# Optimization experiments

Hardware: AMD Instinct MI355X
Metric: run time of the kernel (lower is better)

## Reference

```python
import jax, jax.numpy as jnp
import numpy as np

N = 16384
MUL0, MUL1, MUL2 = 128, 64, 32            # multiplicities of 0e, 1e, 2e
A = 16                                    # node_attr_dim (Ax0e)
D0, D1, D2 = MUL0, MUL1 * 3, MUL2 * 5     # e3nn flat block sizes
DIN = D0 + D1 + D2                        # 480
NGATE = MUL1 + MUL2                       # 96 gate scalars
OUT0 = MUL0 + NGATE                       # 224 scalar (0e) outputs of fctp_1


def setup_inputs() -> dict:
    key = jax.random.key(0)
    ks = jax.random.split(key, 10)
    f32 = jnp.float32
    return {
        "node_vec": jax.random.normal(ks[0], (N, DIN), f32),
        "node_embedding": jax.random.normal(ks[1], (N, A), f32),
        # fctp_1 path weights (fully-connected TP with Ax0e attr)
        "W1_l0": jax.random.normal(ks[2], (MUL0, A, OUT0), f32),
        "W1_l1": jax.random.normal(ks[3], (MUL1, A, MUL1), f32),
        "W1_l2": jax.random.normal(ks[4], (MUL2, A, MUL2), f32),
        "b1": jnp.zeros((OUT0,), f32),
        # fctp_2 scalar-path weight (only 0e x 0e -> 0e path exists)
        "W2": jax.random.normal(ks[5], (MUL0, A, A), f32),
        "b2": jnp.zeros((A,), f32),
        # scalar readout MLP: LinearRS -> SiLU -> LinearRS
        "W3": jax.random.normal(ks[6], (A, A), f32),
        "b3": jnp.zeros((A,), f32),
        "W4": jax.random.normal(ks[7], (A, 1), f32),
        "b4": jnp.zeros((1,), f32),
    }


def reference(node_vec, node_embedding, W1_l0, W1_l1, W1_l2, b1, W2, b2, W3, b3, W4, b4):
    # split e3nn-layout features into per-l blocks [N, mul, 2l+1]
    x0 = node_vec[:, :D0]                               # [N, 128]   l=0
    x1 = node_vec[:, D0:D0 + D1].reshape(-1, MUL1, 3)   # [N, 64, 3] l=1
    x2 = node_vec[:, D0 + D1:].reshape(-1, MUL2, 5)     # [N, 32, 5] l=2
    a = node_embedding                                  # [N, A] 0e scalars
    # fctp_1: fully-connected TP with Ax0e attr -> per-l bilinear mix (path-normalized)
    s = jnp.einsum('ni,na,iak->nk', x0, a, W1_l0) / np.sqrt(MUL0 * A) + b1  # [N, 224]
    y1 = jnp.einsum('nim,na,iak->nkm', x1, a, W1_l1) / np.sqrt(MUL1 * A)    # [N, 64, 3]
    y2 = jnp.einsum('nim,na,iak->nkm', x2, a, W1_l2) / np.sqrt(MUL2 * A)    # [N, 32, 5]
    # SwishGate: SiLU on scalars, sigmoid gates multiply the l>0 channels
    scalars = jax.nn.silu(s[:, :MUL0])
    gates = jax.nn.sigmoid(s[:, MUL0:])
    y1 = y1 * gates[:, :MUL1, None]
    y2 = y2 * gates[:, MUL1:, None]
    # fctp_2: output irreps = Ax0e, so only the 0e x 0e -> 0e path exists;
    # the gated l>0 features have no path to 0e (same as the torch TP).
    mid = jnp.einsum('ni,na,iak->nk', scalars, a, W2) / np.sqrt(MUL0 * A) + b2  # [N, A]
    # output_network: LinearRS -> SiLU -> LinearRS (rescale 1/sqrt(fan_in))
    h = jax.nn.silu(mid @ W3 / np.sqrt(A) + b3)
    return h @ W4 / np.sqrt(A) + b4                     # [N, 1]
```

## Files before the change

kernel.cpp:

```cpp
#include <hip/hip_runtime.h>
#include <hip/hip_bf16.h>


#define NKC 64

typedef _Float16 h8  __attribute__((ext_vector_type(8)));
typedef _Float16 h2  __attribute__((ext_vector_type(2)));
typedef float    f32x4 __attribute__((ext_vector_type(4)));

static __device__ __forceinline__ unsigned int pack2h(float a, float b) {
    h2 t = {(_Float16)a, (_Float16)b};
    return __builtin_bit_cast(unsigned int, t);
}
static __device__ __forceinline__ f32x4 mfma_h(uint4 a, uint4 b, f32x4 c) {
    return __builtin_amdgcn_mfma_f32_16x16x32_f16(
        __builtin_bit_cast(h8, a), __builtin_bit_cast(h8, b), c, 0, 0, 0);
}
static __device__ __forceinline__ uint4 mk_afrag(_Float16 xh, const h2* ee) {
    h2 xx = {xh, xh};
    uint4 r;
    r.x = __builtin_bit_cast(unsigned int, (h2)(xx * ee[0]));
    r.y = __builtin_bit_cast(unsigned int, (h2)(xx * ee[1]));
    r.z = __builtin_bit_cast(unsigned int, (h2)(xx * ee[2]));
    r.w = __builtin_bit_cast(unsigned int, (h2)(xx * ee[3]));
    return r;
}

__global__ __launch_bounds__(256) void prep_kernel(
        const float* __restrict__ W1, const float* __restrict__ W2,
        _Float16* __restrict__ W1T, _Float16* __restrict__ W2T) {
    const int b = blockIdx.x, kc = b >> 2, tp = b & 3;
    const int tid = threadIdx.x;
    __shared__ float l1[32 * 36];
    __shared__ float l2[32 * 20];

    {
        int row = tid >> 3, c4 = tid & 7;
        float4 v = *(const float4*)(W1 + (size_t)(kc * 32 + row) * 224 + tp * 32 + c4 * 4);
        *(float4*)(l1 + row * 36 + c4 * 4) = v;
    }
    if (tp == 0 && tid < 128) {
        int row = tid >> 2, c4 = tid & 3;
        float4 v = *(const float4*)(W2 + (size_t)(kc * 32 + row) * 16 + c4 * 4);
        *(float4*)(l2 + row * 20 + c4 * 4) = v;
    }
    __syncthreads();

    if (tid < 128) {
        int tl = tid >> 6, t = tp * 2 + tl, lane = tid & 63;
        int q = lane >> 4, cc = lane & 15, colL = tl * 16 + cc;
        unsigned int w[4];
#pragma unroll
        for (int jj = 0; jj < 4; ++jj)
            w[jj] = pack2h(l1[(q * 8 + 2 * jj) * 36 + colL],
                           l1[(q * 8 + 2 * jj + 1) * 36 + colL]);
        *(uint4*)(W1T + (size_t)kc * 4096 + (t * 64 + lane) * 8) =
            make_uint4(w[0], w[1], w[2], w[3]);
    }
    if (tp == 0 && tid >= 128 && tid < 192) {
        int lane = tid - 128, q = lane >> 4, cc = lane & 15;
        unsigned int w[4];
#pragma unroll
        for (int jj = 0; jj < 4; ++jj)
            w[jj] = pack2h(l2[(q * 8 + 2 * jj) * 20 + cc],
                           l2[(q * 8 + 2 * jj + 1) * 20 + cc]);
        *(uint4*)(W2T + (size_t)kc * 512 + lane * 8) = make_uint4(w[0], w[1], w[2], w[3]);
    }
}

__global__ __launch_bounds__(1024, 4) void main_kernel(
        const float* __restrict__ node_vec, const float* __restrict__ emb,
        const _Float16* __restrict__ W1T, const _Float16* __restrict__ W2T,
        const float* __restrict__ b1, const float* __restrict__ b2,
        const float* __restrict__ W3, const float* __restrict__ b3,
        const float* __restrict__ W4, const float* __restrict__ b4,
        float* __restrict__ out) {
    const int tid  = threadIdx.x;
    const int wave = tid >> 6, lane = tid & 63;
    const int q = lane >> 4, c = lane & 15;
    const int ihalf = q >> 1;
    const int g = wave >> 2;
    const int cs = wave & 3;
    const int nodeBase = blockIdx.x * 64;

    __shared__ _Float16 x0s[64 * 136];
    __shared__ _Float16 scs[64 * 136];
    __shared__ float    midp[4 * 64 * 17];
    __shared__ float    mids[64 * 17];
    __shared__ float    w3s[256];
    __shared__ float    b3s[16];
    __shared__ float    w4s[16];
    __shared__ float    b4s[1];

    for (int idx = tid; idx < 2048; idx += 1024) {
        int row = idx >> 5, c4 = idx & 31;
        float4 v = *(const float4*)(node_vec + (size_t)(nodeBase + row) * 480 + c4 * 4);
        unsigned int ua = pack2h(v.x, v.y), ub = pack2h(v.z, v.w);
        *(uint2*)(&x0s[row * 136 + c4 * 4]) = make_uint2(ua, ub);
    }
    if (tid < 256) w3s[tid] = W3[tid];
    if (tid < 16) { b3s[tid] = b3[tid]; w4s[tid] = W4[tid]; }
    if (tid == 0) b4s[0] = b4[0];

    h2 ee[4];
    {
        const float* ep = emb + (size_t)(nodeBase + g * 16 + c) * 16 + (q & 1) * 8;
        float4 v0 = *(const float4*)ep;
        float4 v1 = *(const float4*)(ep + 4);
        ee[0] = (h2){(_Float16)v0.x, (_Float16)v0.y};
        ee[1] = (h2){(_Float16)v0.z, (_Float16)v0.w};
        ee[2] = (h2){(_Float16)v1.x, (_Float16)v1.y};
        ee[3] = (h2){(_Float16)v1.z, (_Float16)v1.w};
    }
    __syncthreads();

    f32x4 acc[2];
    acc[0] = (f32x4){0.f, 0.f, 0.f, 0.f};
    acc[1] = (f32x4){0.f, 0.f, 0.f, 0.f};

    const int rowA = g * 16 + c;
    const uint4* bptr = (const uint4*)W1T + lane;
    const int cs2 = cs * 2;

    uint4 bb0[2], bb1[2];
    _Float16 xs0, xs1;
    bb0[0] = bptr[(cs2    ) * 64];
    bb0[1] = bptr[(cs2 + 1) * 64];
    xs0 = x0s[rowA * 136 + ihalf];

    for (int kc = 0; kc < NKC; kc += 2) {
        const int k1 = kc + 1;
        bb1[0] = bptr[(k1 * 8 + cs2    ) * 64];
        bb1[1] = bptr[(k1 * 8 + cs2 + 1) * 64];
        xs1 = x0s[rowA * 136 + 2 * k1 + ihalf];
        {
            uint4 af = mk_afrag(xs0, ee);
            acc[0] = mfma_h(af, bb0[0], acc[0]);
            acc[1] = mfma_h(af, bb0[1], acc[1]);
        }
        const int k2 = (kc + 2 < NKC) ? kc + 2 : 0;
        bb0[0] = bptr[(k2 * 8 + cs2    ) * 64];
        bb0[1] = bptr[(k2 * 8 + cs2 + 1) * 64];
        xs0 = x0s[rowA * 136 + 2 * k2 + ihalf];
        {
            uint4 af = mk_afrag(xs1, ee);
            acc[0] = mfma_h(af, bb1[0], acc[0]);
            acc[1] = mfma_h(af, bb1[1], acc[1]);
        }
    }

    const float inv2048 = 0.022097086912079608f;
#pragma unroll
    for (int tt = 0; tt < 2; ++tt) {
        int t = cs2 + tt;
        float bb1v = b1[t * 16 + c];
#pragma unroll
        for (int r = 0; r < 4; ++r) {
            int node = g * 16 + q * 4 + r;
            float s  = acc[tt][r] * inv2048 + bb1v;
            float sc = s / (1.f + __expf(-s));
            scs[node * 136 + t * 16 + c] = (_Float16)sc;
        }
    }
    __syncthreads();

    {
        const int ks = cs;
        const int rowS = g * 16 + c;
        const uint4* b2p = (const uint4*)W2T + lane;
        f32x4 macc = (f32x4){0.f, 0.f, 0.f, 0.f};
        const int kb = ks * 16;
        uint4 wb0, wb1;
        _Float16 sv0, sv1;
        wb0 = b2p[kb * 64];
        sv0 = scs[rowS * 136 + 2 * kb + ihalf];
        for (int u = 0; u < 16; u += 2) {
            const int kB = kb + u + 1;
            wb1 = b2p[kB * 64];
            sv1 = scs[rowS * 136 + 2 * kB + ihalf];
            macc = mfma_h(mk_afrag(sv0, ee), wb0, macc);
            const int kC = (u + 2 < 16) ? kb + u + 2 : kb;
            wb0 = b2p[kC * 64];
            sv0 = scs[rowS * 136 + 2 * kC + ihalf];
            macc = mfma_h(mk_afrag(sv1, ee), wb1, macc);
        }
#pragma unroll
        for (int r = 0; r < 4; ++r) {
            int node = g * 16 + q * 4 + r;
            midp[(ks * 64 + node) * 17 + c] = macc[r];
        }
    }
    __syncthreads();

    {
        int node = tid >> 4, col = tid & 15;
        float m = midp[node * 17 + col] + midp[(64 + node) * 17 + col]
                + midp[(128 + node) * 17 + col] + midp[(192 + node) * 17 + col];
        mids[node * 17 + col] = m * inv2048 + b2[col];
    }
    __syncthreads();

    {
        int n = tid >> 4, jj = tid & 15;
        float a = 0.f;
#pragma unroll
        for (int cc = 0; cc < 16; ++cc) a += mids[n * 17 + cc] * w3s[cc * 16 + jj];
        a = a * 0.25f + b3s[jj];
        float hh = a / (1.f + __expf(-a));
        float po = hh * w4s[jj];
        po += __shfl_xor(po, 1);
        po += __shfl_xor(po, 2);
        po += __shfl_xor(po, 4);
        po += __shfl_xor(po, 8);
        if (jj == 0) out[nodeBase + n] = po * 0.25f + b4s[0];
    }
}

extern "C" void kernel_launch(void* const* d_in, const int* in_sizes, int n_in,
                              void* d_out, int out_size, void* d_ws, size_t ws_size,
                              hipStream_t stream) {
    const float* node_vec = (const float*)d_in[0];
    const float* emb      = (const float*)d_in[1];
    const float* W1       = (const float*)d_in[2];
    const float* b1v      = (const float*)d_in[5];
    const float* W2       = (const float*)d_in[6];
    const float* b2v      = (const float*)d_in[7];
    const float* W3       = (const float*)d_in[8];
    const float* b3v      = (const float*)d_in[9];
    const float* W4       = (const float*)d_in[10];
    const float* b4v      = (const float*)d_in[11];

    _Float16* W1T = (_Float16*)d_ws;
    _Float16* W2T = W1T + 64 * 4096;
    float* out = (float*)d_out;

    prep_kernel<<<256, 256, 0, stream>>>(W1, W2, W1T, W2T);
    main_kernel<<<256, 1024, 0, stream>>>(node_vec, emb, W1T, W2T,
                                          b1v, b2v, W3, b3v, W4, b4v, out);
}
```

Before: 115.8 us.

## Halve nodes per block, split x0 into even/odd planes, batch weight loads

Blocks now cover 32 nodes with 512 threads, launching 512 blocks to spread work over more CUs. The x0 and scalar tiles in shared memory are split into even/odd-index planes, so each lane reads its A-fragment values as contiguous h4/h8 vector loads instead of scalar halves. The W1 loop now prefetches groups of 8 fragments per stage, and the W2 loop uses a 4-deep rolling prefetch. The cost is more register pressure, plus each W1T chunk is now read by twice as many blocks.

```diff
diff --git a/kernel.cpp b/kernel.cpp
--- a/kernel.cpp
+++ b/kernel.cpp
@@ -1,11 +1,11 @@
 #include <hip/hip_runtime.h>
-#include <hip/hip_bf16.h>
 
 
 #define NKC 64
 
-typedef _Float16 h8  __attribute__((ext_vector_type(8)));
-typedef _Float16 h2  __attribute__((ext_vector_type(2)));
+typedef _Float16 h8 __attribute__((ext_vector_type(8)));
+typedef _Float16 h4 __attribute__((ext_vector_type(4)));
+typedef _Float16 h2 __attribute__((ext_vector_type(2)));
 typedef float    f32x4 __attribute__((ext_vector_type(4)));
 
 static __device__ __forceinline__ unsigned int pack2h(float a, float b) {
@@ -68,7 +68,7 @@
     }
 }
 
-__global__ __launch_bounds__(1024, 4) void main_kernel(
+__global__ __launch_bounds__(512, 4) void main_kernel(
         const float* __restrict__ node_vec, const float* __restrict__ emb,
         const _Float16* __restrict__ W1T, const _Float16* __restrict__ W2T,
         const float* __restrict__ b1, const float* __restrict__ b2,
@@ -78,25 +78,30 @@
     const int tid  = threadIdx.x;
     const int wave = tid >> 6, lane = tid & 63;
     const int q = lane >> 4, c = lane & 15;
-    const int ihalf = q >> 1;
-    const int g = wave >> 2;
-    const int cs = wave & 3;
-    const int nodeBase = blockIdx.x * 64;
-
-    __shared__ _Float16 x0s[64 * 136];
-    __shared__ _Float16 scs[64 * 136];
-    __shared__ float    midp[4 * 64 * 17];
-    __shared__ float    mids[64 * 17];
+    const int ih = q >> 1;
+    const int aodd = q & 1;
+    const int mh = wave >> 2;
+    const int cq = wave & 3;
+    const int nodeBase = blockIdx.x * 32;
+
+    __shared__ _Float16 x0e[32 * 72];
+    __shared__ _Float16 x0o[32 * 72];
+    __shared__ _Float16 sce[32 * 72];
+    __shared__ _Float16 sco[32 * 72];
+    __shared__ float    midp[4 * 32 * 17];
+    __shared__ float    mids[32 * 17];
     __shared__ float    w3s[256];
     __shared__ float    b3s[16];
     __shared__ float    w4s[16];
     __shared__ float    b4s[1];
 
-    for (int idx = tid; idx < 2048; idx += 1024) {
+    for (int idx = tid; idx < 1024; idx += 512) {
         int row = idx >> 5, c4 = idx & 31;
         float4 v = *(const float4*)(node_vec + (size_t)(nodeBase + row) * 480 + c4 * 4);
-        unsigned int ua = pack2h(v.x, v.y), ub = pack2h(v.z, v.w);
-        *(uint2*)(&x0s[row * 136 + c4 * 4]) = make_uint2(ua, ub);
+        h2 ev = {(_Float16)v.x, (_Float16)v.z};
+        h2 ov = {(_Float16)v.y, (_Float16)v.w};
+        *(h2*)(x0e + row * 72 + c4 * 2) = ev;
+        *(h2*)(x0o + row * 72 + c4 * 2) = ov;
     }
     if (tid < 256) w3s[tid] = W3[tid];
     if (tid < 16) { b3s[tid] = b3[tid]; w4s[tid] = W4[tid]; }
@@ -104,7 +109,7 @@
 
     h2 ee[4];
     {
-        const float* ep = emb + (size_t)(nodeBase + g * 16 + c) * 16 + (q & 1) * 8;
+        const float* ep = emb + (size_t)(nodeBase + mh * 16 + c) * 16 + aodd * 8;
         float4 v0 = *(const float4*)ep;
         float4 v1 = *(const float4*)(ep + 4);
         ee[0] = (h2){(_Float16)v0.x, (_Float16)v0.y};
@@ -114,88 +119,92 @@
     }
     __syncthreads();
 
-    f32x4 acc[2];
-    acc[0] = (f32x4){0.f, 0.f, 0.f, 0.f};
-    acc[1] = (f32x4){0.f, 0.f, 0.f, 0.f};
-
-    const int rowA = g * 16 + c;
-    const uint4* bptr = (const uint4*)W1T + lane;
-    const int cs2 = cs * 2;
-
-    uint4 bb0[2], bb1[2];
-    _Float16 xs0, xs1;
-    bb0[0] = bptr[(cs2    ) * 64];
-    bb0[1] = bptr[(cs2 + 1) * 64];
-    xs0 = x0s[rowA * 136 + ihalf];
-
-    for (int kc = 0; kc < NKC; kc += 2) {
-        const int k1 = kc + 1;
-        bb1[0] = bptr[(k1 * 8 + cs2    ) * 64];
-        bb1[1] = bptr[(k1 * 8 + cs2 + 1) * 64];
-        xs1 = x0s[rowA * 136 + 2 * k1 + ihalf];
-        {
-            uint4 af = mk_afrag(xs0, ee);
-            acc[0] = mfma_h(af, bb0[0], acc[0]);
-            acc[1] = mfma_h(af, bb0[1], acc[1]);
+    f32x4 acc0 = (f32x4){0.f, 0.f, 0.f, 0.f};
+    f32x4 acc1 = (f32x4){0.f, 0.f, 0.f, 0.f};
+
+    const uint4* bp = (const uint4*)W1T + cq * 128 + lane;
+    const _Float16* xrow = (ih ? x0o : x0e) + (mh * 16 + c) * 72;
+
+    uint4 B0[8], B1[8];
+    h4 xa, xb;
+
+#define LOADG(B, X, g)                                                         \
+    {                                                                          \
+        _Pragma("unroll")                                                      \
+        for (int u = 0; u < 4; ++u) {                                          \
+            B[2 * u]     = bp[(4 * (g) + u) * 512];                            \
+            B[2 * u + 1] = bp[(4 * (g) + u) * 512 + 64];                       \
+        }                                                                      \
+        X = *(const h4*)(xrow + 4 * (g));                                      \
+    }
+#define DOG(B, X)                                                              \
+    {                                                                          \
+        _Pragma("unroll")                                                      \
+        for (int u = 0; u < 4; ++u) {                                          \
+            uint4 af = mk_afrag(X[u], ee);                                     \
+            acc0 = mfma_h(af, B[2 * u], acc0);                                 \
+            acc1 = mfma_h(af, B[2 * u + 1], acc1);                             \
+        }                                                                      \
+    }
+
+    LOADG(B0, xa, 0);
+    for (int it = 0; it < 8; ++it) {
+        LOADG(B1, xb, 2 * it + 1);
+        DOG(B0, xa);
+        int g2 = (2 * it + 2) & 15;
+        LOADG(B0, xa, g2);
+        DOG(B1, xb);
+    }
+#undef LOADG
+#undef DOG
+
+    const float inv2048 = 0.022097086912079608f;
+#pragma unroll
+    for (int tt = 0; tt < 2; ++tt) {
+        int t = cq * 2 + tt;
+        float bb1v = b1[t * 16 + c];
+        const f32x4& av = tt ? acc1 : acc0;
+        _Float16* dst = (c & 1) ? sco : sce;
+        int colh = t * 8 + (c >> 1);
+#pragma unroll
+        for (int r = 0; r < 4; ++r) {
+            int node = mh * 16 + q * 4 + r;
+            float s  = av[r] * inv2048 + bb1v;
+            float sc = s / (1.f + __expf(-s));
+            dst[node * 72 + colh] = (_Float16)sc;
         }
-        const int k2 = (kc + 2 < NKC) ? kc + 2 : 0;
-        bb0[0] = bptr[(k2 * 8 + cs2    ) * 64];
-        bb0[1] = bptr[(k2 * 8 + cs2 + 1) * 64];
-        xs0 = x0s[rowA * 136 + 2 * k2 + ihalf];
-        {
-            uint4 af = mk_afrag(xs1, ee);
-            acc[0] = mfma_h(af, bb1[0], acc[0]);
-            acc[1] = mfma_h(af, bb1[1], acc[1]);
-        }
-    }
-
-    const float inv2048 = 0.022097086912079608f;
-#pragma unroll
-    for (int tt = 0; tt < 2; ++tt) {
-        int t = cs2 + tt;
-        float bb1v = b1[t * 16 + c];
-#pragma unroll
-        for (int r = 0; r < 4; ++r) {
-            int node = g * 16 + q * 4 + r;
-            float s  = acc[tt][r] * inv2048 + bb1v;
-            float sc = s / (1.f + __expf(-s));
-            scs[node * 136 + t * 16 + c] = (_Float16)sc;
-        }
-    }
-    __syncthreads();
-
-    {
-        const int ks = cs;
-        const int rowS = g * 16 + c;
+    }
+    __syncthreads();
+
+    {
+        const int ks = cq;
+        const _Float16* srow = (ih ? sco : sce) + (mh * 16 + c) * 72 + ks * 16;
+        h8 sx0 = *(const h8*)(srow);
+        h8 sx1 = *(const h8*)(srow + 8);
         const uint4* b2p = (const uint4*)W2T + lane;
         f32x4 macc = (f32x4){0.f, 0.f, 0.f, 0.f};
-        const int kb = ks * 16;
-        uint4 wb0, wb1;
-        _Float16 sv0, sv1;
-        wb0 = b2p[kb * 64];
-        sv0 = scs[rowS * 136 + 2 * kb + ihalf];
-        for (int u = 0; u < 16; u += 2) {
-            const int kB = kb + u + 1;
-            wb1 = b2p[kB * 64];
-            sv1 = scs[rowS * 136 + 2 * kB + ihalf];
-            macc = mfma_h(mk_afrag(sv0, ee), wb0, macc);
-            const int kC = (u + 2 < 16) ? kb + u + 2 : kb;
-            wb0 = b2p[kC * 64];
-            sv0 = scs[rowS * 136 + 2 * kC + ihalf];
-            macc = mfma_h(mk_afrag(sv1, ee), wb1, macc);
+        uint4 wb[4];
+#pragma unroll
+        for (int u = 0; u < 4; ++u) wb[u] = b2p[(ks * 16 + u) * 64];
+#pragma unroll
+        for (int k2 = 0; k2 < 16; ++k2) {
+            uint4 cur = wb[k2 & 3];
+            if (k2 + 4 < 16) wb[k2 & 3] = b2p[(ks * 16 + k2 + 4) * 64];
+            _Float16 sv = (k2 < 8) ? sx0[k2] : sx1[k2 - 8];
+            macc = mfma_h(mk_afrag(sv, ee), cur, macc);
         }
 #pragma unroll
         for (int r = 0; r < 4; ++r) {
-            int node = g * 16 + q * 4 + r;
-            midp[(ks * 64 + node) * 17 + c] = macc[r];
+            int node = mh * 16 + q * 4 + r;
+            midp[(ks * 32 + node) * 17 + c] = macc[r];
         }
     }
     __syncthreads();
 
     {
         int node = tid >> 4, col = tid & 15;
-        float m = midp[node * 17 + col] + midp[(64 + node) * 17 + col]
-                + midp[(128 + node) * 17 + col] + midp[(192 + node) * 17 + col];
+        float m = midp[node * 17 + col] + midp[(32 + node) * 17 + col]
+                + midp[(64 + node) * 17 + col] + midp[(96 + node) * 17 + col];
         mids[node * 17 + col] = m * inv2048 + b2[col];
     }
     __syncthreads();
@@ -235,6 +244,6 @@
     float* out = (float*)d_out;
 
     prep_kernel<<<256, 256, 0, stream>>>(W1, W2, W1T, W2T);
-    main_kernel<<<256, 1024, 0, stream>>>(node_vec, emb, W1T, W2T,
-                                          b1v, b2v, W3, b3v, W4, b4v, out);
-}
+    main_kernel<<<512, 512, 0, stream>>>(node_vec, emb, W1T, W2T,
+                                         b1v, b2v, W3, b3v, W4, b4v, out);
+}
```

New measurement: 116.7 us. About the same (+0.7%).
